# Performance work log

Measured on AMD Instinct MI355X. Metric: run time of the kernel, lower is better.

Reference implementation:

```python
import jax, jax.numpy as jnp
import numpy as np

D_MODEL = 768
D_STATE = 16
D_CONV = 4
EXPAND = 2
D_INNER = EXPAND * D_MODEL  # 1536
DT_RANK = (D_MODEL + 15) // 16  # 48, mamba_ssm default dt_rank='auto'
BATCH = 2
SEQ = 2048


def setup_inputs() -> dict:
    key = jax.random.key(0)
    ks = jax.random.split(key, 9)
    f = lambda k, shp, s=0.02: (jax.random.normal(k, shp, jnp.float32) * s)
    return {
        "x": jax.random.normal(ks[0], (BATCH, SEQ, D_MODEL), jnp.float32),
        "ln_w": jnp.ones((D_MODEL,), jnp.float32),
        "ln_b": jnp.zeros((D_MODEL,), jnp.float32),
        "in_proj_w": f(ks[1], (2 * D_INNER, D_MODEL)),          # no bias (mamba default)
        "conv_w": f(ks[2], (D_INNER, D_CONV), 0.1),              # depthwise causal conv
        "conv_b": f(ks[3], (D_INNER,), 0.1),
        "x_proj_w": f(ks[4], (DT_RANK + 2 * D_STATE, D_INNER)),  # no bias
        "dt_proj_w": f(ks[5], (D_INNER, DT_RANK), 0.1),
        "dt_proj_b": f(ks[6], (D_INNER,), 0.5),
        "A_log": jnp.log(jnp.broadcast_to(
            jnp.arange(1, D_STATE + 1, dtype=jnp.float32), (D_INNER, D_STATE))),  # S4D-real init
        "D": jnp.ones((D_INNER,), jnp.float32),
        "out_proj_w": f(ks[7], (D_MODEL, D_INNER)),              # no bias
    }


def _layernorm(x, w, b, eps=1e-5):
    mu = jnp.mean(x, axis=-1, keepdims=True)
    var = jnp.var(x, axis=-1, keepdims=True)
    return (x - mu) * jax.lax.rsqrt(var + eps) * w + b


def _mamba(xn, in_proj_w, conv_w, conv_b, x_proj_w, dt_proj_w, dt_proj_b,
           A_log, D, out_proj_w):
    B, L, _ = xn.shape
    # input projection -> gate z and ssm branch u
    xz = jnp.einsum("bld,ed->ble", xn, in_proj_w)  # [B,L,2*d_inner]
    u, z = jnp.split(xz, 2, axis=-1)
    # causal depthwise conv1d (kernel D_CONV, left pad D_CONV-1) + SiLU
    up = jnp.pad(u, ((0, 0), (D_CONV - 1, 0), (0, 0)))
    uc = conv_b
    for k in range(D_CONV):  # small fixed tap loop
        uc = uc + conv_w[:, k] * up[:, k:k + L, :]
    uc = jax.nn.silu(uc)  # [B,L,d_inner]
    # data-dependent dt, B, C
    dbl = jnp.einsum("bld,ed->ble", uc, x_proj_w)
    dt, Bm, Cm = jnp.split(dbl, [DT_RANK, DT_RANK + D_STATE], axis=-1)
    delta = jax.nn.softplus(jnp.einsum("blr,dr->bld", dt, dt_proj_w) + dt_proj_b)
    A = -jnp.exp(A_log)  # [d_inner, d_state]

    def step(h, inp):
        u_t, d_t, B_t, C_t = inp  # [B,d_inner],[B,d_inner],[B,d_state],[B,d_state]
        dA = jnp.exp(d_t[..., None] * A)                      # [B,d_inner,d_state]
        h = dA * h + (d_t * u_t)[..., None] * B_t[:, None, :]  # discretized update
        y = jnp.einsum("bds,bs->bd", h, C_t)
        return h, y

    h0 = jnp.zeros((B, D_INNER, D_STATE), xn.dtype)
    xs = (uc.transpose(1, 0, 2), delta.transpose(1, 0, 2),
          Bm.transpose(1, 0, 2), Cm.transpose(1, 0, 2))
    _, ys = jax.lax.scan(step, h0, xs)          # ys: [L,B,d_inner]
    y = ys.transpose(1, 0, 2) + uc * D          # skip connection D*u
    y = y * jax.nn.silu(z)                      # gating
    return jnp.einsum("bld,od->blo", y, out_proj_w)


def reference(x, ln_w, ln_b, in_proj_w, conv_w, conv_b, x_proj_w,
              dt_proj_w, dt_proj_b, A_log, D, out_proj_w):
    xn = _layernorm(x, ln_w, ln_b)
    return x + _mamba(xn, in_proj_w, conv_w, conv_b, x_proj_w,
                      dt_proj_w, dt_proj_b, A_log, D, out_proj_w)
```

## Files before the change

kernel.cpp:

```cpp
#include <hip/hip_runtime.h>
#include <hip/hip_bf16.h>
#include <stdint.h>
#include <math.h>

typedef __hip_bfloat16 bf16;
typedef __attribute__((ext_vector_type(8))) short bf16x8;
typedef __attribute__((ext_vector_type(4))) short s16x4;
typedef __attribute__((ext_vector_type(4))) float f32x4;

#define B_   2
#define L_   2048
#define DM   768
#define DI   1536
#define DS   16
#define M_   (B_ * L_)
#define NC   128
#define LC   (L_ / NC)
#define NSEQ (B_ * DI * DS)
#define KSPLIT 12
#define OSPLIT 4
#define LOG2E  1.44269504088896f
#define NLOG2E (-1.44269504088896f)

#define GLOAD_LDS16(g, l)                                                     \
  __builtin_amdgcn_global_load_lds(                                           \
      (const __attribute__((address_space(1))) void*)(g),                     \
      (__attribute__((address_space(3))) void*)(l), 16, 0, 0)

__device__ inline float bf2f(short s) {
  union { unsigned int u; float f; } c;
  c.u = ((unsigned int)(unsigned short)s) << 16;
  return c.f;
}

__global__ __launch_bounds__(256) void k_prep(
    const float* __restrict__ x, const float* __restrict__ w,
    const float* __restrict__ b, bf16* __restrict__ xnb,
    const float* __restrict__ ipw, const float* __restrict__ xpw,
    const float* __restrict__ dpw, const float* __restrict__ opw,
    bf16* __restrict__ wib, bf16* __restrict__ wxb,
    bf16* __restrict__ wdb, bf16* __restrict__ wob) {
  const int tid = threadIdx.x;
  if (blockIdx.x < M_) {
    const int m = blockIdx.x;
    const float* row = x + (size_t)m * DM;
    float v0 = row[tid], v1 = row[tid + 256], v2 = row[tid + 512];
    float s1 = v0 + v1 + v2;
    float s2 = v0 * v0 + v1 * v1 + v2 * v2;
    for (int mm = 1; mm < 64; mm <<= 1) {
      s1 += __shfl_xor(s1, mm);
      s2 += __shfl_xor(s2, mm);
    }
    __shared__ float r1s[4], r2s[4];
    int wv = tid >> 6, ln = tid & 63;
    if (ln == 0) { r1s[wv] = s1; r2s[wv] = s2; }
    __syncthreads();
    s1 = r1s[0] + r1s[1] + r1s[2] + r1s[3];
    s2 = r2s[0] + r2s[1] + r2s[2] + r2s[3];
    float mu = s1 * (1.f / 768.f);
    float var = s2 * (1.f / 768.f) - mu * mu;
    float rs = rsqrtf(var + 1e-5f);
    bf16* orow = xnb + (size_t)m * DM;
    orow[tid]       = __float2bfloat16((v0 - mu) * rs * w[tid]       + b[tid]);
    orow[tid + 256] = __float2bfloat16((v1 - mu) * rs * w[tid + 256] + b[tid + 256]);
    orow[tid + 512] = __float2bfloat16((v2 - mu) * rs * w[tid + 512] + b[tid + 512]);
    return;
  }
  const int n1 = 3072 * 768;
  const int n2 = 768 * 1536;
  const int n3 = 128 * 1536;
  const int n4 = 1536 * 64;
  const int total4 = (n1 + n2 + n3 + n4) / 4;
  const int stride = 512 * 256;
  for (int i4 = (blockIdx.x - M_) * 256 + tid; i4 < total4; i4 += stride) {
    int i = i4 * 4;
    f32x4 v = {0.f, 0.f, 0.f, 0.f};
    bf16* dst;
    if (i < n1) {
      v = *(const f32x4*)&ipw[i];
      dst = &wib[i];
    } else if (i < n1 + n2) {
      int j = i - n1;
      v = *(const f32x4*)&opw[j];
      dst = &wob[j];
    } else if (i < n1 + n2 + n3) {
      int j = i - n1 - n2;
      int r = j / 1536, c = j - r * 1536;
      if (r < 80) v = *(const f32x4*)&xpw[r * 1536 + c];
      dst = &wxb[j];
    } else {
      int j = i - n1 - n2 - n3;
      int r = j >> 6, c = j & 63;
      if (c < 48) v = *(const f32x4*)&dpw[r * 48 + c];
      dst = &wdb[j];
    }
    bf16 t[4];
#pragma unroll
    for (int k = 0; k < 4; ++k) t[k] = __float2bfloat16(v[k]);
    *(s16x4*)dst = *(const s16x4*)t;
  }
}

__device__ __forceinline__ void g256_stage_half(
    const bf16* __restrict__ g, int base_row, int K, int k0,
    short* lhalf, int wid, int lane) {
#pragma unroll
  for (int q = 0; q < 2; ++q) {
    int row_l = q * 64 + wid * 8 + (lane >> 3);
    int slot = (lane & 7) ^ (lane >> 3);
    GLOAD_LDS16(g + (size_t)(base_row + row_l) * K + k0 + slot * 8,
                lhalf + q * 4096 + wid * 512);
  }
}

__device__ __forceinline__ bf16x8 g256_ld(const short* bufop, int h, int row_l,
                                          int kk, int lane) {
  int kslot = (kk >> 3) + (lane >> 4);
  int off = h * 8192 + row_l * 64 + ((kslot ^ (lane & 7)) << 3);
  return *(const bf16x8*)&bufop[off];
}

__global__ __launch_bounds__(512) void k_gemm256(
    const bf16* __restrict__ A, const bf16* __restrict__ Bw, int K,
    bf16* __restrict__ C, int ldc) {
  __shared__ short lds[4 * 16384];
  short* Abuf0 = lds;
  short* Abuf1 = lds + 16384;
  short* Bbuf0 = lds + 32768;
  short* Bbuf1 = lds + 49152;
  const int tid = threadIdx.x, lane = tid & 63, wid = tid >> 6;
  const int wm_i = wid >> 2, wn_i = wid & 3;

  int bidx = blockIdx.x, bidy = blockIdx.y;
  if (gridDim.x == 12 && gridDim.y == 16) {
    int phys = bidy * 12 + bidx;
    int xcd = phys & 7, i = phys >> 3;
    bidy = (xcd & 3) * 4 + (i / 6);
    bidx = (xcd >> 2) * 6 + (i % 6);
  }
  const int m0 = bidy * 256, n0 = bidx * 256;
  const int NT = K >> 6;

  f32x4 acc[8][4] = {};

  g256_stage_half(A, m0, K, 0, Abuf0, wid, lane);
  g256_stage_half(A, m0 + 128, K, 0, Abuf0 + 8192, wid, lane);
  g256_stage_half(Bw, n0, K, 0, Bbuf0, wid, lane);
  g256_stage_half(Bw, n0 + 128, K, 0, Bbuf0 + 8192, wid, lane);
  g256_stage_half(Bw, n0, K, 64, Bbuf1, wid, lane);
  g256_stage_half(Bw, n0 + 128, K, 64, Bbuf1 + 8192, wid, lane);
  asm volatile("s_waitcnt vmcnt(4)" ::: "memory");
  __builtin_amdgcn_s_barrier();

  for (int t = 0; t < NT; ++t) {
    short* Ab  = (t & 1) ? Abuf1 : Abuf0;
    short* Bb  = (t & 1) ? Bbuf1 : Bbuf0;
    short* Anx = (t & 1) ? Abuf0 : Abuf1;

    bf16x8 bfrag[4][2];

#pragma unroll
    for (int p = 0; p < 4; ++p) {
      if (p == 0) {
#pragma unroll
        for (int nf = 0; nf < 4; ++nf) {
          int row_l = (wn_i & 1) * 64 + nf * 16 + (lane & 15);
          bfrag[nf][0] = g256_ld(Bb, wn_i >> 1, row_l, 0, lane);
          bfrag[nf][1] = g256_ld(Bb, wn_i >> 1, row_l, 32, lane);
        }
      }
      bf16x8 af[2][2];
#pragma unroll
      for (int i = 0; i < 2; ++i) {
        int row_l = (p * 2 + i) * 16 + (lane & 15);
        af[i][0] = g256_ld(Ab, wm_i, row_l, 0, lane);
        af[i][1] = g256_ld(Ab, wm_i, row_l, 32, lane);
      }
      if (p == 0) {
        if (t + 1 < NT) g256_stage_half(A, m0, K, (t + 1) * 64, Anx, wid, lane);
      } else if (p == 1) {
        if (t + 1 < NT) g256_stage_half(A, m0 + 128, K, (t + 1) * 64, Anx + 8192, wid, lane);
      } else if (p == 2) {
        if (t + 2 < NT) g256_stage_half(Bw, n0, K, (t + 2) * 64, Bb, wid, lane);
      } else {
        if (t + 2 < NT) {
          g256_stage_half(Bw, n0 + 128, K, (t + 2) * 64, Bb + 8192, wid, lane);
          asm volatile("s_waitcnt vmcnt(4)" ::: "memory");
        } else {
          asm volatile("s_waitcnt vmcnt(0)" ::: "memory");
        }
      }
      __builtin_amdgcn_s_barrier();
      asm volatile("s_waitcnt lgkmcnt(0)" ::: "memory");
      __builtin_amdgcn_s_setprio(1);
#pragma unroll
      for (int i = 0; i < 2; ++i) {
        int mf = p * 2 + i;
#pragma unroll
        for (int nf = 0; nf < 4; ++nf) {
          acc[mf][nf] = __builtin_amdgcn_mfma_f32_16x16x32_bf16(
              af[i][0], bfrag[nf][0], acc[mf][nf], 0, 0, 0);
          acc[mf][nf] = __builtin_amdgcn_mfma_f32_16x16x32_bf16(
              af[i][1], bfrag[nf][1], acc[mf][nf], 0, 0, 0);
        }
      }
      __builtin_amdgcn_s_setprio(0);
      __builtin_amdgcn_s_barrier();
    }
  }

#pragma unroll
  for (int mf = 0; mf < 8; ++mf) {
    int row = m0 + wm_i * 128 + mf * 16 + ((lane >> 4) << 2);
#pragma unroll
    for (int nf = 0; nf < 4; ++nf) {
      int col = n0 + wn_i * 64 + nf * 16 + (lane & 15);
#pragma unroll
      for (int r = 0; r < 4; ++r)
        C[(size_t)(row + r) * ldc + col] = __float2bfloat16(acc[mf][nf][r]);
    }
  }
}

template <int EPI>
__global__ __launch_bounds__(256) void k_gemm_bt(
    const bf16* __restrict__ A, const bf16* __restrict__ Bw, int M, int N, int K,
    void* __restrict__ Cv, int ldc, const float* __restrict__ aux) {
  __shared__ short As[128 * 64];
  __shared__ short Bs[128 * 64];
  const int tid = threadIdx.x, lane = tid & 63, wv = tid >> 6;

  int bidx = blockIdx.x, bidy = blockIdx.y;
  if (gridDim.z == 1 && (gridDim.y & 7) == 0) {
    const int nx = gridDim.x;
    const int phys = bidy * nx + bidx;
    const int xcd = phys & 7, slot = phys >> 3;
    const int mt_per = gridDim.y >> 3;
    bidy = xcd * mt_per + slot / nx;
    bidx = slot % nx;
  }
  const int m0 = bidy * 128, n0 = bidx * 128;

  const int wm = (wv >> 1) * 64, wn = (wv & 1) * 64;
  const int lrow = lane >> 3, lcol8 = (lane & 7) * 8;
  const int ksl = K / gridDim.z;
  const int koff = ksl * blockIdx.z;

  f32x4 acc[4][4] = {};

  for (int k0 = koff; k0 < koff + ksl; k0 += 64) {
    __syncthreads();
#pragma unroll
    for (int j = 0; j < 4; ++j) {
      int reg = j * 4 + wv;
      int r = reg * 8 + lrow;
      GLOAD_LDS16(A + (size_t)(m0 + r) * K + k0 + lcol8, &As[reg * 8 * 64]);
      GLOAD_LDS16(Bw + (size_t)(n0 + r) * K + k0 + lcol8, &Bs[reg * 8 * 64]);
    }
    asm volatile("s_waitcnt vmcnt(0)" ::: "memory");
    __syncthreads();
#pragma unroll
    for (int kk = 0; kk < 64; kk += 32) {
      bf16x8 af[4], bfr[4];
#pragma unroll
      for (int i = 0; i < 4; ++i)
        af[i] = *(const bf16x8*)&As[(wm + i * 16 + (lane & 15)) * 64 + kk + ((lane >> 4) * 8)];
#pragma unroll
      for (int j = 0; j < 4; ++j)
        bfr[j] = *(const bf16x8*)&Bs[(wn + j * 16 + (lane & 15)) * 64 + kk + ((lane >> 4) * 8)];
#pragma unroll
      for (int i = 0; i < 4; ++i)
#pragma unroll
        for (int j = 0; j < 4; ++j)
          acc[i][j] = __builtin_amdgcn_mfma_f32_16x16x32_bf16(af[i], bfr[j], acc[i][j], 0, 0, 0);
    }
  }

  const size_t zoff = (size_t)blockIdx.z * M * ldc;
#pragma unroll
  for (int i = 0; i < 4; ++i) {
    int row_b = m0 + wm + i * 16 + ((lane >> 4) << 2);
#pragma unroll
    for (int j = 0; j < 4; ++j) {
      int col = n0 + wn + j * 16 + (lane & 15);
#pragma unroll
      for (int r = 0; r < 4; ++r) {
        int row = row_b + r;
        float v = acc[i][j][r];
        if (EPI == 0) {
          ((float*)Cv)[zoff + (size_t)row * ldc + col] = v;
        } else if (EPI == 1) {
          ((bf16*)Cv)[(size_t)row * ldc + col] = __float2bfloat16(v);
        } else if (EPI == 2) {
          float t = v + aux[col];
          float sp = fmaxf(t, 0.f) + __logf(1.f + __expf(-fabsf(t)));
          ((bf16*)Cv)[(size_t)row * ldc + col] = __float2bfloat16(sp);
        } else if (EPI == 3) {
          ((float*)Cv)[(size_t)row * ldc + col] = v + aux[(size_t)row * ldc + col];
        } else {
          ((bf16*)Cv)[zoff + (size_t)row * ldc + col] = __float2bfloat16(v);
        }
      }
    }
  }
}

__global__ __launch_bounds__(256) void k_conv(const bf16* __restrict__ xzb,
                                              const float* __restrict__ cw,
                                              const float* __restrict__ cb,
                                              bf16* __restrict__ ucb) {
  const int idx = blockIdx.x * 256 + threadIdx.x;
  const int mp = idx / (DI / 8);
  const int d8 = (idx - mp * (DI / 8)) * 8;
  const int m0 = mp * 2;
  const int tl = m0 & (L_ - 1);

  float wgt[8][4];
#pragma unroll
  for (int j = 0; j < 8; ++j) {
    f32x4 w4 = *(const f32x4*)&cw[(d8 + j) * 4];
#pragma unroll
    for (int k = 0; k < 4; ++k) wgt[j][k] = w4[k];
  }
  const f32x4* cbv = (const f32x4*)&cb[d8];
  f32x4 cb0 = cbv[0], cb1 = cbv[1];
  float acc0[8], acc1[8];
#pragma unroll
  for (int j = 0; j < 4; ++j) {
    acc0[j] = cb0[j]; acc0[4 + j] = cb1[j];
    acc1[j] = cb0[j]; acc1[4 + j] = cb1[j];
  }

  bf16x8 v[5];
  const bf16x8 z8 = (bf16x8)(short)0;
#pragma unroll
  for (int k = 0; k < 5; ++k) {
    int tt = tl - 3 + k;
    v[k] = (tt >= 0) ? *(const bf16x8*)&xzb[(size_t)(m0 - 3 + k) * 3072 + d8] : z8;
  }
#pragma unroll
  for (int k = 0; k < 4; ++k)
#pragma unroll
    for (int j = 0; j < 8; ++j) {
      acc0[j] += wgt[j][k] * bf2f(v[k][j]);
      acc1[j] += wgt[j][k] * bf2f(v[k + 1][j]);
    }

  bf16 o0[8], o1[8];
#pragma unroll
  for (int j = 0; j < 8; ++j) {
    o0[j] = __float2bfloat16(acc0[j] / (1.f + __expf(-acc0[j])));
    o1[j] = __float2bfloat16(acc1[j] / (1.f + __expf(-acc1[j])));
  }
  *(bf16x8*)&ucb[(size_t)m0 * DI + d8]       = *(bf16x8*)o0;
  *(bf16x8*)&ucb[(size_t)(m0 + 1) * DI + d8] = *(bf16x8*)o1;
}

__global__ __launch_bounds__(256) void k_xred(const bf16* __restrict__ xpart,
                                              float* __restrict__ dbl,
                                              bf16* __restrict__ dtb) {
  const int idx = blockIdx.x * 256 + threadIdx.x;
  const int m = idx >> 7, c = idx & 127;
  float sum = 0.f;
#pragma unroll
  for (int s = 0; s < KSPLIT; ++s)
    sum += __bfloat162float(xpart[(size_t)s * (M_ * 128) + idx]);
  dbl[idx] = sum;
  if (c < 64) dtb[m * 64 + c] = __float2bfloat16(c < 48 ? sum : 0.f);
}

__global__ __launch_bounds__(256) void k_ored(const bf16* __restrict__ op,
                                              const float* __restrict__ x,
                                              float* __restrict__ out) {
  const int i8 = (blockIdx.x * 256 + threadIdx.x) * 8;
  bf16x8 pp[OSPLIT];
#pragma unroll
  for (int s = 0; s < OSPLIT; ++s)
    pp[s] = *(const bf16x8*)&op[(size_t)s * M_ * DM + i8];
  const f32x4* xp = (const f32x4*)&x[i8];
  f32x4 x0 = xp[0], x1 = xp[1];
  f32x4 o0, o1;
#pragma unroll
  for (int j = 0; j < 4; ++j) {
    float a0 = 0.f, a1 = 0.f;
#pragma unroll
    for (int s = 0; s < OSPLIT; ++s) {
      a0 += bf2f(pp[s][j]);
      a1 += bf2f(pp[s][4 + j]);
    }
    o0[j] = x0[j] + a0;
    o1[j] = x1[j] + a1;
  }
  f32x4* outp = (f32x4*)&out[i8];
  outp[0] = o0;
  outp[1] = o1;
}

#define DA_CHAIN(dtval)                                                       \
  float r1 = __builtin_amdgcn_exp2f((dtval) * NLOG2E);                        \
  float r2 = r1 * r1, r3 = r2 * r1, r4 = r2 * r2;                             \
  float r5 = r4 * r1, r6 = r4 * r2, r7 = r4 * r3, r8 = r4 * r4;               \
  float dA[16] = {r1, r2, r3, r4, r5, r6, r7, r8,                             \
                  r8 * r1, r8 * r2, r8 * r3, r8 * r4,                         \
                  r8 * r5, r8 * r6, r8 * r7, r8 * r8};

__global__ __launch_bounds__(256) void k_scan1(
    const bf16* __restrict__ dlt, const bf16* __restrict__ ucb,
    const float* __restrict__ dbl,
    bf16* __restrict__ Qb, float* __restrict__ dts) {
  const int blk = blockIdx.x;
  const int cg = blk % (DI / 256);
  const int ch = (blk / (DI / 256)) % NC;
  const int b  = blk / ((DI / 256) * NC);
  const int d  = cg * 256 + threadIdx.x;
  const int t0 = ch * LC;
  __shared__ float sB[LC][16];
  {
    int t = threadIdx.x >> 4, j = threadIdx.x & 15;
    sB[t][j] = dbl[(size_t)(b * L_ + t0 + t) * 128 + 48 + j];
  }
  const bf16* dp = dlt + (size_t)(b * L_ + t0) * DI + d;
  const bf16* up = ucb + (size_t)(b * L_ + t0) * DI + d;
  float dtv[LC], uv[LC];
#pragma unroll
  for (int t = 0; t < LC; ++t) {
    dtv[t] = __bfloat162float(dp[(size_t)t * DI]);
    uv[t]  = __bfloat162float(up[(size_t)t * DI]);
  }
  float h[16];
#pragma unroll
  for (int s = 0; s < 16; ++s) h[s] = 0.f;
  __syncthreads();
  float dtsum = 0.f;
#pragma unroll
  for (int t = 0; t < LC; ++t) {
    float du = dtv[t] * uv[t];
    dtsum += dtv[t];
    const f32x4* bp = (const f32x4*)&sB[t][0];
    f32x4 Bv[4] = {bp[0], bp[1], bp[2], bp[3]};
    DA_CHAIN(dtv[t]);
#pragma unroll
    for (int s = 0; s < 16; ++s)
      h[s] = dA[s] * h[s] + du * Bv[s >> 2][s & 3];
  }
  size_t base = (size_t)ch * NSEQ + (size_t)(b * DI + d) * DS;
  bf16 qs[16];
#pragma unroll
  for (int s = 0; s < 16; ++s) qs[s] = __float2bfloat16(h[s]);
  *(bf16x8*)&Qb[base]     = *(bf16x8*)&qs[0];
  *(bf16x8*)&Qb[base + 8] = *(bf16x8*)&qs[8];
  dts[(size_t)ch * (B_ * DI) + b * DI + d] = dtsum;
}

__global__ __launch_bounds__(256) void k_scan2(const bf16* __restrict__ Qb,
                                               bf16* __restrict__ Hb,
                                               const float* __restrict__ dts,
                                               const float* __restrict__ A_log) {
  const int gid = blockIdx.x * 256 + threadIdx.x;
  const int bd0 = (blockIdx.x * 256) >> 4;
  __shared__ float sDts[NC][16];
  for (int i = threadIdx.x; i < NC * 16; i += 256) {
    int c = i >> 4, k = i & 15;
    sDts[c][k] = dts[(size_t)c * (B_ * DI) + bd0 + k];
  }
  const float a2 = -__expf(A_log[gid % (DI * DS)]) * LOG2E;
  const int bdl = threadIdx.x >> 4;
  __syncthreads();
  float h = 0.f;
  for (int c0 = 0; c0 < NC; c0 += 16) {
    float q[16];
#pragma unroll
    for (int k = 0; k < 16; ++k)
      q[k] = __bfloat162float(Qb[(size_t)(c0 + k) * NSEQ + gid]);
#pragma unroll
    for (int k = 0; k < 16; ++k) {
      float P = __builtin_amdgcn_exp2f(a2 * sDts[c0 + k][bdl]);
      Hb[(size_t)(c0 + k) * NSEQ + gid] = __float2bfloat16(h);
      h = P * h + q[k];
    }
  }
}

__global__ __launch_bounds__(256) void k_scan3(
    const bf16* __restrict__ dlt, const bf16* __restrict__ ucb,
    const bf16* __restrict__ xzb, const float* __restrict__ dbl,
    const float* __restrict__ Dp,
    const bf16* __restrict__ Hb, bf16* __restrict__ ybf) {
  const int blk = blockIdx.x;
  const int cg = blk % (DI / 256);
  const int ch = (blk / (DI / 256)) % NC;
  const int b  = blk / ((DI / 256) * NC);
  const int d  = cg * 256 + threadIdx.x;
  const int t0 = ch * LC;
  __shared__ float sBC[LC][32];
  for (int i = threadIdx.x; i < LC * 32; i += 256) {
    int t = i >> 5, j = i & 31;
    sBC[t][j] = dbl[(size_t)(b * L_ + t0 + t) * 128 + 48 + j];
  }
  const bf16* dp = dlt + (size_t)(b * L_ + t0) * DI + d;
  const bf16* up = ucb + (size_t)(b * L_ + t0) * DI + d;
  const bf16* zp = xzb + (size_t)(b * L_ + t0) * 3072 + DI + d;
  float dtv[LC], uv[LC], zv[LC];
#pragma unroll
  for (int t = 0; t < LC; ++t) {
    dtv[t] = __bfloat162float(dp[(size_t)t * DI]);
    uv[t]  = __bfloat162float(up[(size_t)t * DI]);
    zv[t]  = __bfloat162float(zp[(size_t)t * 3072]);
  }
  float h[16];
  const bf16* Hp = Hb + (size_t)ch * NSEQ + (size_t)(b * DI + d) * DS;
  bf16x8 h0 = *(const bf16x8*)&Hp[0];
  bf16x8 h1 = *(const bf16x8*)&Hp[8];
#pragma unroll
  for (int s = 0; s < 16; ++s) h[s] = bf2f(s < 8 ? h0[s] : h1[s - 8]);
  const float Dd = Dp[d];
  __syncthreads();
  bf16* yp = ybf + (size_t)(b * L_ + t0) * DI + d;
#pragma unroll
  for (int t = 0; t < LC; ++t) {
    float du = dtv[t] * uv[t];
    const f32x4* bc = (const f32x4*)&sBC[t][0];
    f32x4 Bv[4]  = {bc[0], bc[1], bc[2], bc[3]};
    f32x4 Cv4[4] = {bc[4], bc[5], bc[6], bc[7]};
    DA_CHAIN(dtv[t]);
    float y = 0.f;
#pragma unroll
    for (int s = 0; s < 16; ++s) {
      h[s] = dA[s] * h[s] + du * Bv[s >> 2][s & 3];
      y += h[s] * Cv4[s >> 2][s & 3];
    }
    y += Dd * uv[t];
    float g = zv[t] / (1.f + __expf(-zv[t]));
    yp[(size_t)t * DI] = __float2bfloat16(y * g);
  }
}

extern "C" void kernel_launch(void* const* d_in, const int* in_sizes, int n_in,
                              void* d_out, int out_size, void* d_ws, size_t ws_size,
                              hipStream_t stream) {
  const float* x    = (const float*)d_in[0];
  const float* lnw  = (const float*)d_in[1];
  const float* lnb  = (const float*)d_in[2];
  const float* ipw  = (const float*)d_in[3];
  const float* cw   = (const float*)d_in[4];
  const float* cb   = (const float*)d_in[5];
  const float* xpw  = (const float*)d_in[6];
  const float* dpw  = (const float*)d_in[7];
  const float* dpb  = (const float*)d_in[8];
  const float* alog = (const float*)d_in[9];
  const float* Dp   = (const float*)d_in[10];
  const float* opw  = (const float*)d_in[11];

  char* p = (char*)d_ws;
  auto alloc = [&](size_t bytes) {
    char* r = p;
    p += (bytes + 255) & ~(size_t)255;
    return r;
  };
  bf16* xnb  = (bf16*)alloc((size_t)M_ * DM * 2);
  bf16* wib  = (bf16*)alloc((size_t)3072 * 768 * 2);
  bf16* wxb  = (bf16*)alloc((size_t)128 * 1536 * 2);
  bf16* wdb  = (bf16*)alloc((size_t)1536 * 64 * 2);
  bf16* wob  = (bf16*)alloc((size_t)768 * 1536 * 2);
  bf16* xzb  = (bf16*)alloc((size_t)M_ * 3072 * 2);
  bf16* ucb  = (bf16*)alloc((size_t)M_ * DI * 2);
  float* dbl = (float*)alloc((size_t)M_ * 128 * 4);
  bf16* dtb  = (bf16*)alloc((size_t)M_ * 64 * 2);
  bf16* dlt  = (bf16*)alloc((size_t)M_ * DI * 2);
  bf16* ybf  = (bf16*)alloc((size_t)M_ * DI * 2);
  bf16* Qb   = (bf16*)alloc((size_t)NC * NSEQ * 2);
  bf16* Hb   = (bf16*)alloc((size_t)NC * NSEQ * 2);
  float* dts = (float*)alloc((size_t)NC * B_ * DI * 4);
  bf16* xpart = Qb;
  bf16* opart = Qb;

  k_prep<<<M_ + 512, 256, 0, stream>>>(x, lnw, lnb, xnb, ipw, xpw, dpw, opw,
                                       wib, wxb, wdb, wob);

  dim3 g1(3072 / 256, M_ / 256);
  k_gemm256<<<g1, 512, 0, stream>>>(xnb, wib, 768, xzb, 3072);

  k_conv<<<(M_ / 2) * (DI / 8) / 256, 256, 0, stream>>>(xzb, cw, cb, ucb);

  dim3 g2(1, M_ / 128, KSPLIT);
  k_gemm_bt<4><<<g2, 256, 0, stream>>>(ucb, wxb, M_, 128, 1536, xpart, 128, nullptr);

  k_xred<<<(M_ * 128) / 256, 256, 0, stream>>>(xpart, dbl, dtb);

  dim3 g3(1536 / 128, M_ / 128);
  k_gemm_bt<2><<<g3, 256, 0, stream>>>(dtb, wdb, M_, 1536, 64, dlt, 1536, dpb);

  const int nblk = B_ * NC * (DI / 256);
  k_scan1<<<nblk, 256, 0, stream>>>(dlt, ucb, dbl, Qb, dts);
  k_scan2<<<NSEQ / 256, 256, 0, stream>>>(Qb, Hb, dts, alog);
  k_scan3<<<nblk, 256, 0, stream>>>(dlt, ucb, xzb, dbl, Dp, Hb, ybf);

  dim3 g4(768 / 128, M_ / 128, OSPLIT);
  k_gemm_bt<4><<<g4, 256, 0, stream>>>(ybf, wob, M_, 768, 1536, opart, 768, nullptr);

  k_ored<<<(M_ * DM / 8) / 256, 256, 0, stream>>>(opart, x, (float*)d_out);
}
```

Baseline: 147.5 us.

## Replace split-K partial buffers and reduction kernels with atomic accumulation

The split-K GEMMs for x_proj and out_proj now atomically add fp32 results straight into dbl and the output, instead of writing bf16 partials that separate reduce kernels summed. The prep kernel gains extra blocks that copy x into the output as the residual and zero dbl. A new dt_proj kernel reads fp32 dbl directly, converting it to bf16 in LDS and applying softplus in its epilogue, so the dtb staging buffer is no longer needed. This removes two kernel launches and the partial-buffer traffic, at the cost of atomic contention and nondeterministic summation order.

```diff
diff --git a/kernel.cpp b/kernel.cpp
--- a/kernel.cpp
+++ b/kernel.cpp
@@ -39,7 +39,8 @@
     const float* __restrict__ ipw, const float* __restrict__ xpw,
     const float* __restrict__ dpw, const float* __restrict__ opw,
     bf16* __restrict__ wib, bf16* __restrict__ wxb,
-    bf16* __restrict__ wdb, bf16* __restrict__ wob) {
+    bf16* __restrict__ wdb, bf16* __restrict__ wob,
+    float* __restrict__ dout, float* __restrict__ dbl) {
   const int tid = threadIdx.x;
   if (blockIdx.x < M_) {
     const int m = blockIdx.x;
@@ -66,38 +67,56 @@
     orow[tid + 512] = __float2bfloat16((v2 - mu) * rs * w[tid + 512] + b[tid + 512]);
     return;
   }
-  const int n1 = 3072 * 768;
-  const int n2 = 768 * 1536;
-  const int n3 = 128 * 1536;
-  const int n4 = 1536 * 64;
-  const int total4 = (n1 + n2 + n3 + n4) / 4;
-  const int stride = 512 * 256;
-  for (int i4 = (blockIdx.x - M_) * 256 + tid; i4 < total4; i4 += stride) {
-    int i = i4 * 4;
-    f32x4 v = {0.f, 0.f, 0.f, 0.f};
-    bf16* dst;
-    if (i < n1) {
-      v = *(const f32x4*)&ipw[i];
-      dst = &wib[i];
-    } else if (i < n1 + n2) {
-      int j = i - n1;
-      v = *(const f32x4*)&opw[j];
-      dst = &wob[j];
-    } else if (i < n1 + n2 + n3) {
-      int j = i - n1 - n2;
-      int r = j / 1536, c = j - r * 1536;
-      if (r < 80) v = *(const f32x4*)&xpw[r * 1536 + c];
-      dst = &wxb[j];
-    } else {
-      int j = i - n1 - n2 - n3;
-      int r = j >> 6, c = j & 63;
-      if (c < 48) v = *(const f32x4*)&dpw[r * 48 + c];
-      dst = &wdb[j];
-    }
-    bf16 t[4];
-#pragma unroll
-    for (int k = 0; k < 4; ++k) t[k] = __float2bfloat16(v[k]);
-    *(s16x4*)dst = *(const s16x4*)t;
+  if (blockIdx.x < M_ + 512) {
+    const int n1 = 3072 * 768;
+    const int n2 = 768 * 1536;
+    const int n3 = 128 * 1536;
+    const int n4 = 1536 * 64;
+    const int total4 = (n1 + n2 + n3 + n4) / 4;
+    const int stride = 512 * 256;
+    for (int i4 = (blockIdx.x - M_) * 256 + tid; i4 < total4; i4 += stride) {
+      int i = i4 * 4;
+      f32x4 v = {0.f, 0.f, 0.f, 0.f};
+      bf16* dst;
+      if (i < n1) {
+        v = *(const f32x4*)&ipw[i];
+        dst = &wib[i];
+      } else if (i < n1 + n2) {
+        int j = i - n1;
+        v = *(const f32x4*)&opw[j];
+        dst = &wob[j];
+      } else if (i < n1 + n2 + n3) {
+        int j = i - n1 - n2;
+        int r = j / 1536, c = j - r * 1536;
+        if (r < 80) v = *(const f32x4*)&xpw[r * 1536 + c];
+        dst = &wxb[j];
+      } else {
+        int j = i - n1 - n2 - n3;
+        int r = j >> 6, c = j & 63;
+        if (c < 48) v = *(const f32x4*)&dpw[r * 48 + c];
+        dst = &wdb[j];
+      }
+      bf16 t[4];
+#pragma unroll
+      for (int k = 0; k < 4; ++k) t[k] = __float2bfloat16(v[k]);
+      *(s16x4*)dst = *(const s16x4*)t;
+    }
+    return;
+  }
+  if (blockIdx.x < M_ + 512 + 1536) {
+    int i8 = ((blockIdx.x - M_ - 512) * 256 + tid) * 8;
+    const f32x4* src = (const f32x4*)&x[i8];
+    f32x4* dst = (f32x4*)&dout[i8];
+    dst[0] = src[0];
+    dst[1] = src[1];
+    return;
+  }
+  {
+    int i8 = ((blockIdx.x - M_ - 512 - 1536) * 256 + tid) * 8;
+    f32x4 z = {0.f, 0.f, 0.f, 0.f};
+    f32x4* dst = (f32x4*)&dbl[i8];
+    dst[0] = z;
+    dst[1] = z;
   }
 }
 
@@ -276,7 +295,6 @@
     }
   }
 
-  const size_t zoff = (size_t)blockIdx.z * M * ldc;
 #pragma unroll
   for (int i = 0; i < 4; ++i) {
     int row_b = m0 + wm + i * 16 + ((lane >> 4) << 2);
@@ -287,19 +305,90 @@
       for (int r = 0; r < 4; ++r) {
         int row = row_b + r;
         float v = acc[i][j][r];
-        if (EPI == 0) {
-          ((float*)Cv)[zoff + (size_t)row * ldc + col] = v;
-        } else if (EPI == 1) {
+        if (EPI == 1) {
           ((bf16*)Cv)[(size_t)row * ldc + col] = __float2bfloat16(v);
-        } else if (EPI == 2) {
-          float t = v + aux[col];
-          float sp = fmaxf(t, 0.f) + __logf(1.f + __expf(-fabsf(t)));
-          ((bf16*)Cv)[(size_t)row * ldc + col] = __float2bfloat16(sp);
-        } else if (EPI == 3) {
-          ((float*)Cv)[(size_t)row * ldc + col] = v + aux[(size_t)row * ldc + col];
         } else {
-          ((bf16*)Cv)[zoff + (size_t)row * ldc + col] = __float2bfloat16(v);
+          atomicAdd(&((float*)Cv)[(size_t)row * ldc + col], v);
         }
+      }
+    }
+  }
+}
+
+__global__ __launch_bounds__(256) void k_dtproj(
+    const float* __restrict__ dbl, const bf16* __restrict__ Bw,
+    const float* __restrict__ bias, bf16* __restrict__ dlt) {
+  __shared__ short As[128 * 64];
+  __shared__ short Bs[128 * 64];
+  const int tid = threadIdx.x, lane = tid & 63, wv = tid >> 6;
+
+  int bidx = blockIdx.x, bidy = blockIdx.y;
+  {
+    const int nx = gridDim.x;
+    const int phys = bidy * nx + bidx;
+    const int xcd = phys & 7, slot = phys >> 3;
+    const int mt_per = gridDim.y >> 3;
+    bidy = xcd * mt_per + slot / nx;
+    bidx = slot % nx;
+  }
+  const int m0 = bidy * 128, n0 = bidx * 128;
+  const int wm = (wv >> 1) * 64, wn = (wv & 1) * 64;
+  const int lrow = lane >> 3, lcol8 = (lane & 7) * 8;
+
+  {
+    int row = tid >> 1, h = tid & 1;
+    const float* srcp = dbl + (size_t)(m0 + row) * 128 + h * 32;
+    bf16 tmp[32];
+#pragma unroll
+    for (int q = 0; q < 8; ++q) {
+      int c = h * 32 + q * 4;
+      f32x4 v4 = {0.f, 0.f, 0.f, 0.f};
+      if (c < 48) v4 = *(const f32x4*)&srcp[q * 4];
+#pragma unroll
+      for (int e = 0; e < 4; ++e) tmp[q * 4 + e] = __float2bfloat16(v4[e]);
+    }
+#pragma unroll
+    for (int q = 0; q < 4; ++q)
+      *(bf16x8*)&As[row * 64 + h * 32 + q * 8] = *(bf16x8*)&tmp[q * 8];
+  }
+#pragma unroll
+  for (int j = 0; j < 4; ++j) {
+    int reg = j * 4 + wv;
+    int r = reg * 8 + lrow;
+    GLOAD_LDS16(Bw + (size_t)(n0 + r) * 64 + lcol8, &Bs[reg * 8 * 64]);
+  }
+  asm volatile("s_waitcnt vmcnt(0)" ::: "memory");
+  __syncthreads();
+
+  f32x4 acc[4][4] = {};
+#pragma unroll
+  for (int kk = 0; kk < 64; kk += 32) {
+    bf16x8 af[4], bfr[4];
+#pragma unroll
+    for (int i = 0; i < 4; ++i)
+      af[i] = *(const bf16x8*)&As[(wm + i * 16 + (lane & 15)) * 64 + kk + ((lane >> 4) * 8)];
+#pragma unroll
+    for (int j = 0; j < 4; ++j)
+      bfr[j] = *(const bf16x8*)&Bs[(wn + j * 16 + (lane & 15)) * 64 + kk + ((lane >> 4) * 8)];
+#pragma unroll
+    for (int i = 0; i < 4; ++i)
+#pragma unroll
+      for (int j = 0; j < 4; ++j)
+        acc[i][j] = __builtin_amdgcn_mfma_f32_16x16x32_bf16(af[i], bfr[j], acc[i][j], 0, 0, 0);
+  }
+
+#pragma unroll
+  for (int i = 0; i < 4; ++i) {
+    int row_b = m0 + wm + i * 16 + ((lane >> 4) << 2);
+#pragma unroll
+    for (int j = 0; j < 4; ++j) {
+      int col = n0 + wn + j * 16 + (lane & 15);
+      float bs = bias[col];
+#pragma unroll
+      for (int r = 0; r < 4; ++r) {
+        float t = acc[i][j][r] + bs;
+        float sp = fmaxf(t, 0.f) + __logf(1.f + __expf(-fabsf(t)));
+        dlt[(size_t)(row_b + r) * DI + col] = __float2bfloat16(sp);
       }
     }
   }
@@ -354,46 +443,6 @@
   }
   *(bf16x8*)&ucb[(size_t)m0 * DI + d8]       = *(bf16x8*)o0;
   *(bf16x8*)&ucb[(size_t)(m0 + 1) * DI + d8] = *(bf16x8*)o1;
-}
-
-__global__ __launch_bounds__(256) void k_xred(const bf16* __restrict__ xpart,
-                                              float* __restrict__ dbl,
-                                              bf16* __restrict__ dtb) {
-  const int idx = blockIdx.x * 256 + threadIdx.x;
-  const int m = idx >> 7, c = idx & 127;
-  float sum = 0.f;
-#pragma unroll
-  for (int s = 0; s < KSPLIT; ++s)
-    sum += __bfloat162float(xpart[(size_t)s * (M_ * 128) + idx]);
-  dbl[idx] = sum;
-  if (c < 64) dtb[m * 64 + c] = __float2bfloat16(c < 48 ? sum : 0.f);
-}
-
-__global__ __launch_bounds__(256) void k_ored(const bf16* __restrict__ op,
-                                              const float* __restrict__ x,
-                                              float* __restrict__ out) {
-  const int i8 = (blockIdx.x * 256 + threadIdx.x) * 8;
-  bf16x8 pp[OSPLIT];
-#pragma unroll
-  for (int s = 0; s < OSPLIT; ++s)
-    pp[s] = *(const bf16x8*)&op[(size_t)s * M_ * DM + i8];
-  const f32x4* xp = (const f32x4*)&x[i8];
-  f32x4 x0 = xp[0], x1 = xp[1];
-  f32x4 o0, o1;
-#pragma unroll
-  for (int j = 0; j < 4; ++j) {
-    float a0 = 0.f, a1 = 0.f;
-#pragma unroll
-    for (int s = 0; s < OSPLIT; ++s) {
-      a0 += bf2f(pp[s][j]);
-      a1 += bf2f(pp[s][4 + j]);
-    }
-    o0[j] = x0[j] + a0;
-    o1[j] = x1[j] + a1;
-  }
-  f32x4* outp = (f32x4*)&out[i8];
-  outp[0] = o0;
-  outp[1] = o1;
 }
 
 #define DA_CHAIN(dtval)                                                       \
@@ -565,17 +614,15 @@
   bf16* xzb  = (bf16*)alloc((size_t)M_ * 3072 * 2);
   bf16* ucb  = (bf16*)alloc((size_t)M_ * DI * 2);
   float* dbl = (float*)alloc((size_t)M_ * 128 * 4);
-  bf16* dtb  = (bf16*)alloc((size_t)M_ * 64 * 2);
   bf16* dlt  = (bf16*)alloc((size_t)M_ * DI * 2);
   bf16* ybf  = (bf16*)alloc((size_t)M_ * DI * 2);
   bf16* Qb   = (bf16*)alloc((size_t)NC * NSEQ * 2);
   bf16* Hb   = (bf16*)alloc((size_t)NC * NSEQ * 2);
   float* dts = (float*)alloc((size_t)NC * B_ * DI * 4);
-  bf16* xpart = Qb;
-  bf16* opart = Qb;
-
-  k_prep<<<M_ + 512, 256, 0, stream>>>(x, lnw, lnb, xnb, ipw, xpw, dpw, opw,
-                                       wib, wxb, wdb, wob);
+
+  k_prep<<<M_ + 512 + 1536 + 256, 256, 0, stream>>>(
+      x, lnw, lnb, xnb, ipw, xpw, dpw, opw, wib, wxb, wdb, wob,
+      (float*)d_out, dbl);
 
   dim3 g1(3072 / 256, M_ / 256);
   k_gemm256<<<g1, 512, 0, stream>>>(xnb, wib, 768, xzb, 3072);
@@ -583,12 +630,10 @@
   k_conv<<<(M_ / 2) * (DI / 8) / 256, 256, 0, stream>>>(xzb, cw, cb, ucb);
 
   dim3 g2(1, M_ / 128, KSPLIT);
-  k_gemm_bt<4><<<g2, 256, 0, stream>>>(ucb, wxb, M_, 128, 1536, xpart, 128, nullptr);
-
-  k_xred<<<(M_ * 128) / 256, 256, 0, stream>>>(xpart, dbl, dtb);
+  k_gemm_bt<5><<<g2, 256, 0, stream>>>(ucb, wxb, M_, 128, 1536, dbl, 128, nullptr);
 
   dim3 g3(1536 / 128, M_ / 128);
-  k_gemm_bt<2><<<g3, 256, 0, stream>>>(dtb, wdb, M_, 1536, 64, dlt, 1536, dpb);
+  k_dtproj<<<g3, 256, 0, stream>>>(dbl, wdb, dpb, dlt);
 
   const int nblk = B_ * NC * (DI / 256);
   k_scan1<<<nblk, 256, 0, stream>>>(dlt, ucb, dbl, Qb, dts);
@@ -596,7 +641,5 @@
   k_scan3<<<nblk, 256, 0, stream>>>(dlt, ucb, xzb, dbl, Dp, Hb, ybf);
 
   dim3 g4(768 / 128, M_ / 128, OSPLIT);
-  k_gemm_bt<4><<<g4, 256, 0, stream>>>(ybf, wob, M_, 768, 1536, opart, 768, nullptr);
-
-  k_ored<<<(M_ * DM / 8) / 256, 256, 0, stream>>>(opart, x, (float*)d_out);
-}
+  k_gemm_bt<5><<<g4, 256, 0, stream>>>(ybf, wob, M_, 768, 1536, (float*)d_out, 768, nullptr);
+}
```

Result: slower. 186.5 us (+26.4%).
